# Kernel tuning notes

Measured on AMD Instinct MI355X. Metric: run time of the kernel, lower is better.

The kernel has to match this reference:

```python
import jax, jax.numpy as jnp
import numpy as np

N, IN_DIM, HIDDEN, OUT_DIM, K = 16384, 64, 128, 128, 32


def setup_inputs() -> dict:
    key = jax.random.key(0)
    k1, k2, k3 = jax.random.split(key, 3)
    x = jax.random.normal(k1, (N, IN_DIM), dtype=jnp.float32)
    std1 = 1.0 / np.sqrt(2 * IN_DIM)
    w = jax.random.uniform(k2, (HIDDEN, 2 * IN_DIM), dtype=jnp.float32, minval=-std1, maxval=std1)
    std2 = 1.0 / np.sqrt(IN_DIM + HIDDEN)
    w2 = jax.random.uniform(k3, (OUT_DIM, IN_DIM + HIDDEN), dtype=jnp.float32, minval=-std2, maxval=std2)
    return {"x": x, "w": w, "w2": w2, "k": K}


def reference(x, w, w2, k):
    # kNN graph via squared euclidean distances (same ordering as torch.norm cdist)
    sq = jnp.sum(x * x, axis=-1)                      # (N,)
    d2 = sq[:, None] + sq[None, :] - 2.0 * (x @ x.T)  # (N, N)
    _, graph = jax.lax.top_k(-d2, k)                  # (N, k) indices of k smallest distances
    # gather neighbor features and concat broadcast self features
    nb = x[graph]                                      # (N, k, in_dim)
    self_rep = jnp.broadcast_to(x[:, None, :], nb.shape)
    feat = jnp.concatenate([nb, self_rep], axis=-1)    # (N, k, 2*in_dim)
    # linear + Hardtanh + average pooling over neighborhood
    h = jnp.clip(jnp.einsum('nkf,hf->nkh', feat, w), -1.0, 1.0)
    pooled = h.mean(axis=1)                            # (N, hidden)
    # second linear on [pooled, x]
    out = jnp.concatenate([pooled, x], axis=-1) @ w2.T # (N, out_dim)
    return out
```

## Files before the change

### kernel.cpp

```cpp
#include <hip/hip_runtime.h>

#define NPTS   16384
#define IN_DIM 64
#define HID    128
#define KSEL   32

#define CAP      64
#define TRIG     48
#define WIN_HI   44
#define SLACK_FIX 160u
#define DMAX_FIX 0x3FFFFu

typedef _Float16 f16x8 __attribute__((ext_vector_type(8)));
typedef float    f32x4 __attribute__((ext_vector_type(4)));
typedef unsigned short u16;
typedef unsigned int   u32;
typedef unsigned long long u64;
#define INFBITS 0x7f800000u

__global__ __launch_bounds__(256) void prep_kernel(const float* __restrict__ x,
                                                   float* __restrict__ sq,
                                                   u16* __restrict__ ph,
                                                   u16* __restrict__ pl) {
    const int i  = blockIdx.x * 256 + threadIdx.x;
    const int ct = i >> 4, li = i & 15;
    const float4* xr = (const float4*)(x + (size_t)i * IN_DIM);
    float s = 0.f;
#pragma unroll
    for (int c = 0; c < 8; ++c) {
        float4 a = xr[2 * c], b = xr[2 * c + 1];
        float e[8] = {a.x, a.y, a.z, a.w, b.x, b.y, b.z, b.w};
        u32 hw[8], lw[8];
#pragma unroll
        for (int j = 0; j < 8; ++j) {
            s += e[j] * e[j];
            _Float16 h = (_Float16)e[j];
            float hf = (float)h;
            _Float16 l = (_Float16)(e[j] - hf);
            hw[j] = __builtin_bit_cast(u16, h);
            lw[j] = __builtin_bit_cast(u16, l);
        }
        size_t off = ((size_t)ct * 8 + c) * 128 + (size_t)li * 8;
        *(uint4*)(ph + off) = make_uint4(hw[0] | (hw[1] << 16), hw[2] | (hw[3] << 16),
                                         hw[4] | (hw[5] << 16), hw[6] | (hw[7] << 16));
        *(uint4*)(pl + off) = make_uint4(lw[0] | (lw[1] << 16), lw[2] | (lw[3] << 16),
                                         lw[4] | (lw[5] << 16), lw[6] | (lw[7] << 16));
    }
    sq[i] = s;
}

__global__ __launch_bounds__(512, 8) void knn_kernel(const float* __restrict__ x,
                                                     const u16* __restrict__ ph,
                                                     const u16* __restrict__ pl,
                                                     const float* __restrict__ sq,
                                                     int* __restrict__ graph) {
    __shared__ u32 cand[8][16][CAP];
    __shared__ int bcnt[8][16];
    __shared__ u32 bthrU[16];

    const int t = threadIdx.x, lane = t & 63, wave = t >> 6;
    const int g = lane >> 4, li = lane & 15;
    const int rg = blockIdx.x;
    const int rbase = rg * 16;

    if (t < 128) bcnt[t >> 4][t & 15] = 0;
    if (t < 16)  bthrU[t] = 0xffffffffu;

    f16x8 ah[2], al[2];
#pragma unroll
    for (int kh = 0; kh < 2; ++kh) {
        size_t o = ((size_t)rg * 2 + kh) * 512 + (size_t)lane * 8;
        ah[kh] = *(const f16x8*)(ph + o);
        al[kh] = *(const f16x8*)(pl + o);
    }
    float sar[4];
#pragma unroll
    for (int r = 0; r < 4; ++r) sar[r] = sq[rbase + g * 4 + r];
    __syncthreads();

    int ct = wave;
    f16x8 cb0, cb1; float csb;
    {
        size_t o = (size_t)ct * 1024 + (size_t)lane * 8;
        cb0 = *(const f16x8*)(ph + o);
        cb1 = *(const f16x8*)(ph + o + 512);
        csb = sq[ct * 16 + li];
    }

    for (int i = 0; i < 128; ++i) {
        const int nct = ct + 8;
        f16x8 nb0, nb1; float nsb = 0.f;
        if (i < 127) {
            size_t o = (size_t)nct * 1024 + (size_t)lane * 8;
            nb0 = *(const f16x8*)(ph + o);
            nb1 = *(const f16x8*)(ph + o + 512);
            nsb = sq[nct * 16 + li];
        }
        f32x4 a = {0.f, 0.f, 0.f, 0.f};
        a = __builtin_amdgcn_mfma_f32_16x16x32_f16(ah[0], cb0, a, 0, 0, 0);
        a = __builtin_amdgcn_mfma_f32_16x16x32_f16(ah[1], cb1, a, 0, 0, 0);
        a = __builtin_amdgcn_mfma_f32_16x16x32_f16(al[0], cb0, a, 0, 0, 0);
        a = __builtin_amdgcn_mfma_f32_16x16x32_f16(al[1], cb1, a, 0, 0, 0);

        uint4 tu = *(const uint4*)&bthrU[g * 4];
        const u32 thrk[4] = {tu.x, tu.y, tu.z, tu.w};
        const u32 colid = (u32)(ct * 16 + li);
#pragma unroll
        for (int r = 0; r < 4; ++r) {
            float d = fmaxf(fmaf(-2.f, a[r], sar[r] + csb), 0.f);
            u32 dfix = (u32)fminf(d * 512.0f, 262143.0f);
            u32 key = (dfix << 14) | colid;
            bool pred = key <= thrk[r];
            if (__any(pred)) {
                if (pred) {
                    int row = g * 4 + r;
                    int pos = atomicAdd(&bcnt[wave][row], 1);
                    if (pos < CAP) cand[wave][row][pos] = key;
                }
            }
        }
        u64 need = __ballot((lane < 16) && (bcnt[wave][lane] > TRIG));
        while (need) {
            int rr = __ffsll((long long)need) - 1;
            need &= need - 1;
            int n = bcnt[wave][rr]; n = n < CAP ? n : CAP;
            u32 k0 = (lane < n) ? cand[wave][rr][lane] : 0xffffffffu;
            u32 d0 = k0 >> 14;
            u32 lo = 0, hi = bthrU[rr] >> 14, ans = hi;
            for (int it = 0; it < 18 && lo < hi; ++it) {
                u32 mid = lo + ((hi - lo) >> 1);
                int c = __popcll(__ballot(d0 <= mid));
                if (c < 32) lo = mid + 1;
                else { hi = mid; ans = mid; if (c <= WIN_HI) break; }
            }
            u32 ansd = ans + SLACK_FIX; ansd = ansd < DMAX_FIX ? ansd : DMAX_FIX;
            bool keep = d0 <= ansd;
            u64 bal = __ballot(keep);
            int pos = __popcll(bal & ((1ull << lane) - 1ull));
            if (keep) cand[wave][rr][pos] = k0;
            if (lane == 0) {
                bcnt[wave][rr] = __popcll(bal);
                atomicMin(&bthrU[rr], (ansd << 14) | 0x3fffu);
            }
        }
        ct = nct; cb0 = nb0; cb1 = nb1; csb = nsb;
    }

    __syncthreads();

    const u64 mlt = (1ull << lane) - 1ull;
    for (int ii = 0; ii < 2; ++ii) {
        const int lr = wave * 2 + ii;
        const int gr = rbase + lr;
        const float sqa = sq[gr];
        const float4* xa = (const float4*)(x + (size_t)gr * IN_DIM);
        u32 db[8]; int jj[8];
#pragma unroll
        for (int s8 = 0; s8 < 8; ++s8) {
            int nsl = bcnt[s8][lr]; nsl = nsl < CAP ? nsl : CAP;
            u32 dbits = INFBITS; int j = 0;
            if (nsl > 0) {
                if (lane < nsl) {
                    j = (int)(cand[s8][lr][lane] & 0x3fffu);
                    const float4* xb = (const float4*)(x + (size_t)j * IN_DIM);
                    float dot = 0.f;
#pragma unroll
                    for (int q = 0; q < 16; ++q) {
                        float4 av = xa[q], bv = xb[q];
                        dot += av.x * bv.x + av.y * bv.y + av.z * bv.z + av.w * bv.w;
                    }
                    float d = fmaxf(fmaf(-2.f, dot, sqa + sq[j]), 0.f);
                    dbits = __float_as_uint(d);
                }
            }
            db[s8] = dbits; jj[s8] = j;
        }
        u32 lo = 0, hi = INFBITS, ans = hi;
        for (int it = 0; it < 32 && lo < hi; ++it) {
            u32 mid = lo + ((hi - lo) >> 1);
            int c = 0;
#pragma unroll
            for (int s8 = 0; s8 < 8; ++s8)
                c += __popcll(__ballot(db[s8] <= mid));
            if (c < 32) lo = mid + 1;
            else { hi = mid; ans = mid; if (c == 32) break; }
        }
        bool tie[8]; int c_le = 0;
#pragma unroll
        for (int s8 = 0; s8 < 8; ++s8) {
            tie[s8] = (db[s8] == ans);
            c_le += __popcll(__ballot(db[s8] <= ans));
        }
        int extra = c_le - 32;
        while (extra > 0) {
            int mx = -1;
#pragma unroll
            for (int s8 = 0; s8 < 8; ++s8) if (tie[s8] && jj[s8] > mx) mx = jj[s8];
#pragma unroll
            for (int off = 32; off > 0; off >>= 1) {
                int o = __shfl_xor(mx, off); mx = mx > o ? mx : o;
            }
#pragma unroll
            for (int s8 = 0; s8 < 8; ++s8) if (tie[s8] && jj[s8] == mx) tie[s8] = false;
            --extra;
        }
        int* gp = graph + (size_t)gr * KSEL;
        int base = 0;
#pragma unroll
        for (int s8 = 0; s8 < 8; ++s8) {
            bool k = (db[s8] < ans) || tie[s8];
            u64 b = __ballot(k);
            if (k) gp[base + __popcll(b & mlt)] = jj[s8];
            base += __popcll(b);
        }
    }
}

__global__ __launch_bounds__(384) void xw_kernel(const float* __restrict__ x,
                                                 const float* __restrict__ w,
                                                 const float* __restrict__ w2,
                                                 float* __restrict__ XWa,
                                                 float* __restrict__ XWb,
                                                 float* __restrict__ outb) {
    __shared__ float xs[64][64];
    const int t = threadIdx.x;
    const int rbase = blockIdx.x * 64;

    for (int idx = t; idx < 64 * 16; idx += 384) {
        int r = idx >> 4, q = idx & 15;
        ((float4*)xs[r])[q] = ((const float4*)(x + (size_t)(rbase + r) * IN_DIM))[q];
    }
    const int kind = t >> 7;
    const int idx  = t & 127;
    const float* wp = (kind == 0) ? (w + (size_t)idx * 128)
                    : (kind == 1) ? (w + (size_t)idx * 128 + 64)
                                  : (w2 + (size_t)idx * 192 + 128);
    float4 wreg[16];
#pragma unroll
    for (int q = 0; q < 16; ++q) wreg[q] = ((const float4*)wp)[q];
    __syncthreads();

    for (int r = 0; r < 64; ++r) {
        float acc = 0.f;
#pragma unroll
        for (int q = 0; q < 16; ++q) {
            float4 xv = ((float4*)xs[r])[q];
            acc += xv.x * wreg[q].x + xv.y * wreg[q].y +
                   xv.z * wreg[q].z + xv.w * wreg[q].w;
        }
        size_t o = (size_t)(rbase + r) * 128 + idx;
        if (kind == 0)      XWa[o]  = acc;
        else if (kind == 1) XWb[o]  = acc;
        else                outb[o] = acc;
    }
}

__global__ __launch_bounds__(256) void pool_kernel(const int* __restrict__ graph,
                                                   const float* __restrict__ XWa,
                                                   const float* __restrict__ XWb,
                                                   float* __restrict__ pooled) {
    const int t = threadIdx.x, lane = t & 63, wave = t >> 6;
    const int row = blockIdx.x * 4 + wave;
    int gi = graph[(size_t)row * KSEL + (lane & 31)];
    float2 b = ((const float2*)(XWb + (size_t)row * HID))[lane];
    float2 acc = {0.f, 0.f};
#pragma unroll
    for (int c = 0; c < KSEL; ++c) {
        int j = __shfl(gi, c);
        float2 v = ((const float2*)(XWa + (size_t)j * HID))[lane];
        acc.x += fminf(fmaxf(v.x + b.x, -1.f), 1.f);
        acc.y += fminf(fmaxf(v.y + b.y, -1.f), 1.f);
    }
    float2* pr = (float2*)(pooled + (size_t)row * HID);
    pr[lane] = make_float2(acc.x * (1.f / 32.f), acc.y * (1.f / 32.f));
}

__global__ __launch_bounds__(256) void out_kernel(const float* __restrict__ pooled,
                                                  const float* __restrict__ w2,
                                                  float* __restrict__ out) {
    __shared__ float ws2[128][132];
    __shared__ float pt[64][128];
    const int t = threadIdx.x;
    const int rbase = blockIdx.x * 64;

    for (int idx = t; idx < 128 * 32; idx += 256) {
        int o = idx >> 5, q = idx & 31;
        ((float4*)&ws2[o][0])[q] = ((const float4*)(w2 + (size_t)o * 192))[q];
    }
    for (int idx = t; idx < 64 * 32; idx += 256) {
        int r = idx >> 5, q = idx & 31;
        ((float4*)&pt[r][0])[q] = ((const float4*)(pooled + (size_t)(rbase + r) * 128))[q];
    }
    __syncthreads();

    const int o = t & 127, rsub = t >> 7;
    for (int rp = 0; rp < 32; ++rp) {
        int r = rp * 2 + rsub;
        float acc = 0.f;
#pragma unroll
        for (int q = 0; q < 32; ++q) {
            float4 pv = ((float4*)&pt[r][0])[q];
            float4 wv = ((float4*)&ws2[o][0])[q];
            acc += pv.x * wv.x + pv.y * wv.y + pv.z * wv.z + pv.w * wv.w;
        }
        size_t off = (size_t)(rbase + r) * 128 + o;
        out[off] += acc;
    }
}

extern "C" void kernel_launch(void* const* d_in, const int* in_sizes, int n_in,
                              void* d_out, int out_size, void* d_ws, size_t ws_size,
                              hipStream_t stream) {
    const float* x  = (const float*)d_in[0];
    const float* w  = (const float*)d_in[1];
    const float* w2 = (const float*)d_in[2];
    float* out = (float*)d_out;

    float* sq     = (float*)d_ws;
    int*   graph  = (int*)(sq + NPTS);
    float* XWa    = (float*)(graph + (size_t)NPTS * KSEL);
    float* XWb    = XWa + (size_t)NPTS * HID;
    float* region = XWb + (size_t)NPTS * HID;
    u16*   ph     = (u16*)region;
    u16*   pl     = ph + (size_t)NPTS * IN_DIM;
    float* pooled = region;

    prep_kernel<<<NPTS / 256, 256, 0, stream>>>(x, sq, ph, pl);
    knn_kernel<<<NPTS / 16, 512, 0, stream>>>(x, ph, pl, sq, graph);
    xw_kernel<<<NPTS / 64, 384, 0, stream>>>(x, w, w2, XWa, XWb, out);
    pool_kernel<<<NPTS / 4, 256, 0, stream>>>(graph, XWa, XWb, pooled);
    out_kernel<<<NPTS / 64, 256, 0, stream>>>(pooled, w2, out);
}
```

Baseline: 761.7 us.

## Enlarge kNN candidate buffers and aggregate per-group candidate atomics

Raises the per-row candidate buffer from 64 to 96 entries with a higher compaction trigger, so the ballot/binary-search compaction runs less often. The compaction and the final exact re-ranking now handle two 64-lane slices per row. Candidate insertion now does one atomicAdd per 16-lane group with ballot prefix offsets, instead of one atomic per lane. The cost is more LDS for the candidate arrays, which may lower occupancy, and double the exact-distance and selection work in the final phase.

```diff
diff --git a/kernel.cpp b/kernel.cpp
--- a/kernel.cpp
+++ b/kernel.cpp
@@ -5,9 +5,9 @@
 #define HID    128
 #define KSEL   32
 
-#define CAP      64
-#define TRIG     48
-#define WIN_HI   44
+#define CAP      96
+#define TRIG     80
+#define WIN_HI   40
 #define SLACK_FIX 160u
 #define DMAX_FIX 0x3FFFFu
 
@@ -111,10 +111,17 @@
             u32 dfix = (u32)fminf(d * 512.0f, 262143.0f);
             u32 key = (dfix << 14) | colid;
             bool pred = key <= thrk[r];
-            if (__any(pred)) {
+            u64 bal = __ballot(pred);
+            if (bal) {
+                const int row = g * 4 + r;
+                u32 balg = (u32)(bal >> (g * 16)) & 0xFFFFu;
+                int cnt = __popc(balg);
+                int src = g * 16 + (__ffs(balg) - 1);
+                int base = 0;
+                if (cnt && lane == src) base = atomicAdd(&bcnt[wave][row], cnt);
+                base = __shfl(base, src);
                 if (pred) {
-                    int row = g * 4 + r;
-                    int pos = atomicAdd(&bcnt[wave][row], 1);
+                    int pos = base + __popc(balg & ((1u << li) - 1u));
                     if (pos < CAP) cand[wave][row][pos] = key;
                 }
             }
@@ -125,21 +132,26 @@
             need &= need - 1;
             int n = bcnt[wave][rr]; n = n < CAP ? n : CAP;
             u32 k0 = (lane < n) ? cand[wave][rr][lane] : 0xffffffffu;
-            u32 d0 = k0 >> 14;
+            u32 k1 = (lane < 32 && 64 + lane < n) ? cand[wave][rr][64 + lane]
+                                                  : 0xffffffffu;
+            u32 d0 = k0 >> 14, d1 = k1 >> 14;
             u32 lo = 0, hi = bthrU[rr] >> 14, ans = hi;
             for (int it = 0; it < 18 && lo < hi; ++it) {
                 u32 mid = lo + ((hi - lo) >> 1);
-                int c = __popcll(__ballot(d0 <= mid));
+                int c = __popcll(__ballot(d0 <= mid)) +
+                        __popcll(__ballot(d1 <= mid));
                 if (c < 32) lo = mid + 1;
                 else { hi = mid; ans = mid; if (c <= WIN_HI) break; }
             }
             u32 ansd = ans + SLACK_FIX; ansd = ansd < DMAX_FIX ? ansd : DMAX_FIX;
-            bool keep = d0 <= ansd;
-            u64 bal = __ballot(keep);
-            int pos = __popcll(bal & ((1ull << lane) - 1ull));
-            if (keep) cand[wave][rr][pos] = k0;
+            bool kp0 = d0 <= ansd, kp1 = d1 <= ansd;
+            u64 b0 = __ballot(kp0), b1 = __ballot(kp1);
+            u64 mlt = (1ull << lane) - 1ull;
+            if (kp0) cand[wave][rr][__popcll(b0 & mlt)] = k0;
+            int c0 = __popcll(b0);
+            if (kp1) cand[wave][rr][c0 + __popcll(b1 & mlt)] = k1;
             if (lane == 0) {
-                bcnt[wave][rr] = __popcll(bal);
+                bcnt[wave][rr] = c0 + __popcll(b1);
                 atomicMin(&bthrU[rr], (ansd << 14) | 0x3fffu);
             }
         }
@@ -154,14 +166,18 @@
         const int gr = rbase + lr;
         const float sqa = sq[gr];
         const float4* xa = (const float4*)(x + (size_t)gr * IN_DIM);
-        u32 db[8]; int jj[8];
-#pragma unroll
-        for (int s8 = 0; s8 < 8; ++s8) {
-            int nsl = bcnt[s8][lr]; nsl = nsl < CAP ? nsl : CAP;
+        int ns[8];
+#pragma unroll
+        for (int s = 0; s < 8; ++s) { int v = bcnt[s][lr]; ns[s] = v < CAP ? v : CAP; }
+        u32 db[16]; int jj[16];
+#pragma unroll
+        for (int s16 = 0; s16 < 16; ++s16) {
+            const int sl = s16 >> 1;
+            const int off = (s16 & 1) * 64 + lane;
             u32 dbits = INFBITS; int j = 0;
-            if (nsl > 0) {
-                if (lane < nsl) {
-                    j = (int)(cand[s8][lr][lane] & 0x3fffu);
+            if (ns[sl] > (s16 & 1) * 64) {
+                if (off < ns[sl]) {
+                    j = (int)(cand[sl][lr][off] & 0x3fffu);
                     const float4* xb = (const float4*)(x + (size_t)j * IN_DIM);
                     float dot = 0.f;
 #pragma unroll
@@ -173,44 +189,44 @@
                     dbits = __float_as_uint(d);
                 }
             }
-            db[s8] = dbits; jj[s8] = j;
+            db[s16] = dbits; jj[s16] = j;
         }
         u32 lo = 0, hi = INFBITS, ans = hi;
         for (int it = 0; it < 32 && lo < hi; ++it) {
             u32 mid = lo + ((hi - lo) >> 1);
             int c = 0;
 #pragma unroll
-            for (int s8 = 0; s8 < 8; ++s8)
-                c += __popcll(__ballot(db[s8] <= mid));
+            for (int s16 = 0; s16 < 16; ++s16)
+                c += __popcll(__ballot(db[s16] <= mid));
             if (c < 32) lo = mid + 1;
             else { hi = mid; ans = mid; if (c == 32) break; }
         }
-        bool tie[8]; int c_le = 0;
-#pragma unroll
-        for (int s8 = 0; s8 < 8; ++s8) {
-            tie[s8] = (db[s8] == ans);
-            c_le += __popcll(__ballot(db[s8] <= ans));
+        bool tie[16]; int c_le = 0;
+#pragma unroll
+        for (int s16 = 0; s16 < 16; ++s16) {
+            tie[s16] = (db[s16] == ans);
+            c_le += __popcll(__ballot(db[s16] <= ans));
         }
         int extra = c_le - 32;
         while (extra > 0) {
             int mx = -1;
 #pragma unroll
-            for (int s8 = 0; s8 < 8; ++s8) if (tie[s8] && jj[s8] > mx) mx = jj[s8];
+            for (int s16 = 0; s16 < 16; ++s16) if (tie[s16] && jj[s16] > mx) mx = jj[s16];
 #pragma unroll
             for (int off = 32; off > 0; off >>= 1) {
                 int o = __shfl_xor(mx, off); mx = mx > o ? mx : o;
             }
 #pragma unroll
-            for (int s8 = 0; s8 < 8; ++s8) if (tie[s8] && jj[s8] == mx) tie[s8] = false;
+            for (int s16 = 0; s16 < 16; ++s16) if (tie[s16] && jj[s16] == mx) tie[s16] = false;
             --extra;
         }
         int* gp = graph + (size_t)gr * KSEL;
         int base = 0;
 #pragma unroll
-        for (int s8 = 0; s8 < 8; ++s8) {
-            bool k = (db[s8] < ans) || tie[s8];
+        for (int s16 = 0; s16 < 16; ++s16) {
+            bool k = (db[s16] < ans) || tie[s16];
             u64 b = __ballot(k);
-            if (k) gp[base + __popcll(b & mlt)] = jj[s8];
+            if (k) gp[base + __popcll(b & mlt)] = jj[s16];
             base += __popcll(b);
         }
     }
```

After: 809.4 us. 1.06x slower.
